# Optimization experiments

Hardware: AMD Instinct MI355X
Metric: run time of the kernel (lower is better)

## Reference

```python
import jax, jax.numpy as jnp
import numpy as np

B, T, C, H, W = 16, 8, 16, 64, 64
HID = 32          # round(sqrt(num_audio_input_ch * num_latent_ch)) = sqrt(16*64)
LAT = 64          # num_latent_ch
K = 3             # kernel_size


def conv(x, w, b):
    # x: [B,Cin,H,W], w: [Cout,Cin,K,K] (OIHW), SAME padding == padding (1,1) for 3x3
    y = jax.lax.conv_general_dilated(x, w, (1, 1), 'SAME',
                                     dimension_numbers=('NCHW', 'OIHW', 'NCHW'))
    return y + b[None, :, None, None]


def lstm_scan(x_seq, w, b, hid):
    # x_seq: [T,B,Cin,H,W] -> hidden sequence [T,B,hid,H,W]
    Bn, Hh, Ww = x_seq.shape[1], x_seq.shape[3], x_seq.shape[4]
    h0 = jnp.zeros((Bn, hid, Hh, Ww), x_seq.dtype)

    def step(carry, x_t):
        h, c = carry
        z = conv(jnp.concatenate([x_t, h], axis=1), w, b)     # [B,4*hid,H,W]
        i, f, o, g = jnp.split(z, 4, axis=1)                   # gate order i,f,o,g
        c2 = jax.nn.sigmoid(f) * c + jax.nn.sigmoid(i) * jnp.tanh(g)
        h2 = jax.nn.sigmoid(o) * jnp.tanh(c2)
        return (h2, c2), h2

    _, hs = jax.lax.scan(step, (h0, h0), x_seq)
    return hs


def bidir_layer(x_seq, wf, bf, wb, bb, hid):
    hf = lstm_scan(x_seq, wf, bf, hid)
    hb = jnp.flip(lstm_scan(jnp.flip(x_seq, 0), wb, bb, hid), 0)
    return jnp.concatenate([hf, hb], axis=2)                   # [T,B,2*hid,H,W]


def setup_inputs() -> dict:
    key = jax.random.key(0)
    ks = jax.random.split(key, 16)
    s = 0.05
    pe_dim = C * H * W
    inp = {
        'x_audio': jax.random.normal(ks[0], (B, T, C, H, W), jnp.float32),
        'midi_notes': jax.random.uniform(ks[1], (B, T, 2), jnp.float32, 0.0, 127.0),
        # note encoder: Linear(2,4) -> ReLU -> Linear(4, C*H*W) -> Tanh
        'enc_w1': jax.random.normal(ks[2], (2, 4), jnp.float32) * s,
        'enc_b1': jnp.zeros((4,), jnp.float32),
        'enc_w2': jax.random.normal(ks[3], (4, pe_dim), jnp.float32) * s,
        'enc_b2': jnp.zeros((pe_dim,), jnp.float32),
        # layer 0 (input C=16), fwd + bwd cells
        'w0f': jax.random.normal(ks[4], (4 * HID, C + HID, K, K), jnp.float32) * s,
        'b0f': jnp.zeros((4 * HID,), jnp.float32),
        'w0b': jax.random.normal(ks[5], (4 * HID, C + HID, K, K), jnp.float32) * s,
        'b0b': jnp.zeros((4 * HID,), jnp.float32),
        # layer 1 (input 2*HID=64)
        'w1f': jax.random.normal(ks[6], (4 * HID, 2 * HID + HID, K, K), jnp.float32) * s,
        'b1f': jnp.zeros((4 * HID,), jnp.float32),
        'w1b': jax.random.normal(ks[7], (4 * HID, 2 * HID + HID, K, K), jnp.float32) * s,
        'b1b': jnp.zeros((4 * HID,), jnp.float32),
        # final conv: 2*HID -> LAT
        'fc_w': jax.random.normal(ks[8], (LAT, 2 * HID, K, K), jnp.float32) * s,
        'fc_b': jnp.zeros((LAT,), jnp.float32),
    }
    return inp


def reference(x_audio, midi_notes, enc_w1, enc_b1, enc_w2, enc_b2,
              w0f, b0f, w0b, b0b, w1f, b1f, w1b, b1b, fc_w, fc_b):
    # positional encoding from MIDI notes, vectorized over all timesteps
    notes = -0.5 + midi_notes / 64.0                              # [B,T,2]
    pe = jnp.tanh(jax.nn.relu(notes @ enc_w1 + enc_b1) @ enc_w2 + enc_b2)  # [B,T,C*H*W]
    x = x_audio + pe.reshape(x_audio.shape)
    xs = jnp.transpose(x, (1, 0, 2, 3, 4))                        # [T,B,C,H,W]
    h = bidir_layer(xs, w0f, b0f, w0b, b0b, HID)                  # [T,B,64,H,W]
    h = bidir_layer(h, w1f, b1f, w1b, b1b, HID)                   # [T,B,64,H,W]
    return conv(h[-1], fc_w, fc_b)                                # [B,LAT,H,W]
```

## Files before the change

kernel.cpp:

```cpp
#include <hip/hip_runtime.h>

typedef _Float16 f16;
typedef _Float16 f16x8 __attribute__((ext_vector_type(8)));
typedef float f32x16 __attribute__((ext_vector_type(16)));

namespace {

constexpr int B_ = 16, T_ = 8, HW = 4096;

__device__ __forceinline__ float sigm(float x)  { return 1.f / (1.f + __expf(-x)); }
__device__ __forceinline__ float ftanh(float x) { return 1.f - 2.f / (1.f + __expf(2.f * x)); }

__device__ __forceinline__ f32x16 zero16() {
  f32x16 v;
#pragma unroll
  for (int i = 0; i < 16; ++i) v[i] = 0.f;
  return v;
}

__device__ __forceinline__ f16x8 zero8h() {
  f16x8 v;
#pragma unroll
  for (int i = 0; i < 8; ++i) v[i] = (f16)0.f;
  return v;
}

struct WSet { const float* src; f16* dst; int KC, NCO, CIN; };

__global__ void warr_kernel(WSet s0, WSet s1, WSet s2, WSet s3, WSet s4) {
  WSet s = s0;
  switch (blockIdx.y) { case 1: s = s1; break; case 2: s = s2; break;
                        case 3: s = s3; break; case 4: s = s4; break; default: break; }
  int n = 9 * s.KC * s.NCO * 16;
  int i = blockIdx.x * 256 + threadIdx.x;
  if (i >= n) return;
  int kk = i & 15;
  int t = i >> 4;
  int co = t % s.NCO;
  int dkc = t / s.NCO;
  int kc = dkc % s.KC, dydx = dkc / s.KC;
  int ci = kc * 16 + kk;
  float v = (ci < s.CIN) ? s.src[(co * s.CIN + ci) * 9 + dydx] : 0.f;
  s.dst[i] = (f16)v;
}

__global__ void pe_kernel(const float* __restrict__ xa, const float* __restrict__ midi,
                          const float* __restrict__ w1, const float* __restrict__ b1,
                          const float* __restrict__ w2, const float* __restrict__ b2,
                          f16* __restrict__ xs) {
  int gid = blockIdx.x * 256 + threadIdx.x;
  int half = gid & 1;
  int gpx = gid >> 1;
  int bt = gpx >> 12, gp = gpx & 4095;
  float n0 = -0.5f + midi[bt * 2 + 0] * (1.f / 64.f);
  float n1 = -0.5f + midi[bt * 2 + 1] * (1.f / 64.f);
  float hk[4];
#pragma unroll
  for (int k = 0; k < 4; ++k)
    hk[k] = fmaxf(fmaf(n0, w1[k], fmaf(n1, w1[4 + k], b1[k])), 0.f);
  f16x8 ov;
#pragma unroll
  for (int j = 0; j < 8; ++j) {
    int c = half * 8 + j;
    long p = (long)c * HW + gp;
    float z = b2[p];
#pragma unroll
    for (int k = 0; k < 4; ++k) z = fmaf(hk[k], w2[(long)k * 65536 + p], z);
    ov[j] = (f16)(xa[(long)bt * 65536 + p] + ftanh(z));
  }
  *reinterpret_cast<f16x8*>(xs + (long)gpx * 16 + half * 8) = ov;
}

struct ConvDir {
  const f16* x;  long xbs;
  const f16* h;  long hbs;
  const f16* w;
  const float* bias;
  const f16* cin;
  f16* cout;
  float* fout;
  f16* hout; long hobs;
};

template<int CIN1, int CIN2, int CINPAD, int KCF, int KC, int HST, int HOST,
         bool GATES, int NCO, int MG>
__global__ __launch_bounds__(512, 4)
void conv_mfma(ConvDir p0, ConvDir p1)
{
  constexpr int NG = 8 / MG;
  constexpr int NF = NCO / (NG * 32);
  constexpr int NPH = 9 * KC;
  constexpr int ACT_BYTES = 180 * CINPAD * 2;
  constexpr int ZB_BYTES  = GATES ? 128 * 128 * 2 : 0;
  constexpr int SMEM = ACT_BYTES > ZB_BYTES ? ACT_BYTES : ZB_BYTES;
  __shared__ __align__(16) char smem[SMEM];
  f16* act = (f16*)smem;
  f16* zls = (f16*)smem;

  const ConvDir P = blockIdx.y ? p1 : p0;
  const int b = blockIdx.z;
  const int tileY = blockIdx.x >> 2, tileX = blockIdx.x & 3;
  const int gy0 = tileY * 8, gx0 = tileX * 16;
  const int tid = threadIdx.x;

  const int lane = tid & 63, wv = tid >> 6;
  const int mg = wv % MG, ng = wv / MG;
  const int rl = lane & 31;
  const int khalf = (lane >> 5) * 8;
  const int laneA = ((rl >> 4) * 18 + (rl & 15)) * CINPAD + khalf;
  const int laneB = rl * 16 + khalf;
  const f16* __restrict__ wng = P.w + laneB + (long)ng * NF * 32 * 16;
  const f16* __restrict__ arow = act + laneA;

  constexpr int UPX = CIN1 / 8, UPH = CIN2 / 8, UPP = UPX + UPH;
  constexpr int NU  = 180 * UPP;
  constexpr int PER = (NU + 511) / 512;
  const bool have_h = (P.h != nullptr);
  f16x8 sreg[PER];
#pragma unroll
  for (int p = 0; p < PER; ++p) {
    sreg[p] = zero8h();
    int i = tid + p * 512;
    if (i < NU) {
      int px = i / UPP, u = i - px * UPP;
      int py = px / 18, pxx = px - py * 18;
      int gy = gy0 + py - 1, gx = gx0 + pxx - 1;
      if ((unsigned)gy < 64u && (unsigned)gx < 64u && (u < UPX || have_h)) {
        long gp = (long)gy * 64 + gx;
        const f16* src = (u < UPX) ? (P.x + b * P.xbs + gp * CIN1 + u * 8)
                                   : (P.h + b * P.hbs + gp * HST + (u - UPX) * 8);
        sreg[p] = *reinterpret_cast<const f16x8*>(src);
      }
    }
  }

  f16x8 bfr[2][NF];
  f16x8 afr[2];

  auto LBF = [&](int ph) {
    const int slot = ph & 1;
    const int dydx = ph / KC, kc = ph % KC;
#pragma unroll
    for (int nf = 0; nf < NF; ++nf)
      bfr[slot][nf] = *reinterpret_cast<const f16x8*>(
          wng + ((long)(dydx * KCF + kc) * NCO + nf * 32) * 16);
  };
  auto LAF = [&](int ph) {
    const int slot = ph & 1;
    const int dydx = ph / KC, kc = ph % KC;
    const int dy = dydx / 3, dx = dydx % 3;
    afr[slot] = *reinterpret_cast<const f16x8*>(
        arow + dx * CINPAD + ((mg * 2 + dy) * 18) * CINPAD + kc * 16);
  };

  LBF(0);
  if (NPH > 1) LBF(1);

#pragma unroll
  for (int p = 0; p < PER; ++p) {
    int i = tid + p * 512;
    if (i < NU) {
      int px = i / UPP, u = i - px * UPP;
      *reinterpret_cast<f16x8*>(act + px * CINPAD + u * 8) = sreg[p];
    }
  }
  __syncthreads();

  f32x16 acc[NF];
#pragma unroll
  for (int nf = 0; nf < NF; ++nf) acc[nf] = zero16();

  LAF(0);
#pragma unroll
  for (int ph = 0; ph < NPH; ++ph) {
    const int slot = ph & 1;
    if (ph + 1 < NPH) LAF(ph + 1);
#pragma unroll
    for (int nf = 0; nf < NF; ++nf)
      acc[nf] = __builtin_amdgcn_mfma_f32_32x32x16_f16(afr[slot], bfr[slot][nf], acc[nf], 0, 0, 0);
    if (ph + 2 < NPH) LBF(ph + 2);
  }

  __syncthreads();

  if constexpr (GATES) {
#pragma unroll
    for (int nf = 0; nf < NF; ++nf) {
      const int col = (ng * NF + nf) * 32 + rl;
      const float bs = P.bias[col];
#pragma unroll
      for (int r = 0; r < 16; ++r) {
        int row = (r & 3) + 8 * (r >> 2) + 4 * (lane >> 5);
        zls[(mg * 32 + row) * 128 + col] = (f16)(acc[nf][r] + bs);
      }
    }
    __syncthreads();
    const int q = tid & 3, px = tid >> 2;
    const int py = px >> 4, pxx = px & 15;
    const long gp = (long)(gy0 + py) * 64 + (gx0 + pxx);
    const f16* zb = zls + px * 128 + q * 8;
    f16x8 zi8 = *reinterpret_cast<const f16x8*>(zb);
    f16x8 zf8 = *reinterpret_cast<const f16x8*>(zb + 32);
    f16x8 zo8 = *reinterpret_cast<const f16x8*>(zb + 64);
    f16x8 zg8 = *reinterpret_cast<const f16x8*>(zb + 96);
    const long cbase = ((long)b * HW + gp) * 32 + q * 8;
    f16x8 c8 = P.cin ? *reinterpret_cast<const f16x8*>(P.cin + cbase) : zero8h();
    f16x8 c2v, h2v;
#pragma unroll
    for (int j = 0; j < 8; ++j) {
      float c2 = sigm((float)zf8[j]) * (float)c8[j]
               + sigm((float)zi8[j]) * ftanh((float)zg8[j]);
      c2v[j] = (f16)c2;
      h2v[j] = (f16)(sigm((float)zo8[j]) * ftanh(c2));
    }
    if (P.cout) *reinterpret_cast<f16x8*>(P.cout + cbase) = c2v;
    *reinterpret_cast<f16x8*>(P.hout + b * P.hobs + gp * HOST + q * 8) = h2v;
  } else {
#pragma unroll
    for (int nf = 0; nf < NF; ++nf) {
      const int co = (ng * NF + nf) * 32 + rl;
      const float bs = P.bias[co];
#pragma unroll
      for (int r = 0; r < 16; ++r) {
        int row = (r & 3) + 8 * (r >> 2) + 4 * (lane >> 5);
        int pxt = mg * 32 + row;
        int py = pxt >> 4, pxx = pxt & 15;
        long gp = (long)(gy0 + py) * 64 + (gx0 + pxx);
        P.fout[((long)b * NCO + co) * HW + gp] = acc[nf][r] + bs;
      }
    }
  }
}

}

extern "C" void kernel_launch(void* const* d_in, const int* in_sizes, int n_in,
                              void* d_out, int out_size, void* d_ws, size_t ws_size,
                              hipStream_t stream) {
  const float* x_audio = (const float*)d_in[0];
  const float* midi    = (const float*)d_in[1];
  const float* enc_w1  = (const float*)d_in[2];
  const float* enc_b1  = (const float*)d_in[3];
  const float* enc_w2  = (const float*)d_in[4];
  const float* enc_b2  = (const float*)d_in[5];
  const float* w0f = (const float*)d_in[6];
  const float* b0f = (const float*)d_in[7];
  const float* w0b = (const float*)d_in[8];
  const float* b0b = (const float*)d_in[9];
  const float* w1f = (const float*)d_in[10];
  const float* b1f = (const float*)d_in[11];
  const float* w1b = (const float*)d_in[12];
  const float* b1b = (const float*)d_in[13];
  const float* fcw = (const float*)d_in[14];
  const float* fcb = (const float*)d_in[15];

  char* ws = (char*)d_ws;
  size_t off = 0;
  auto alloc = [&](size_t bytes) { char* p = ws + off; off += (bytes + 255) & ~(size_t)255; return p; };

  f16* xs    = (f16*)alloc((size_t)B_ * T_ * HW * 16 * 2);
  f16* seq0  = (f16*)alloc((size_t)T_ * B_ * HW * 64 * 2);
  f16* c0f   = (f16*)alloc((size_t)B_ * HW * 32 * 2);
  f16* c0b   = (f16*)alloc((size_t)B_ * HW * 32 * 2);
  f16* c1f   = (f16*)alloc((size_t)B_ * HW * 32 * 2);
  f16* h1p0  = (f16*)alloc((size_t)B_ * HW * 32 * 2);
  f16* h1p1  = (f16*)alloc((size_t)B_ * HW * 32 * 2);
  f16* h1bw  = (f16*)alloc((size_t)B_ * HW * 32 * 2);
  f16* wt0f  = (f16*)alloc((size_t)9 * 3 * 128 * 16 * 2);
  f16* wt0b  = (f16*)alloc((size_t)9 * 3 * 128 * 16 * 2);
  f16* wt1f  = (f16*)alloc((size_t)9 * 6 * 128 * 16 * 2);
  f16* wt1b  = (f16*)alloc((size_t)9 * 6 * 128 * 16 * 2);
  f16* wtfc  = (f16*)alloc((size_t)9 * 4 * 64 * 16 * 2);

  {
    WSet s0{w0f, wt0f, 3, 128, 48}, s1{w0b, wt0b, 3, 128, 48};
    WSet s2{w1f, wt1f, 6, 128, 96}, s3{w1b, wt1b, 6, 128, 96};
    WSet s4{fcw, wtfc, 4, 64, 64};
    warr_kernel<<<dim3(432, 5), 256, 0, stream>>>(s0, s1, s2, s3, s4);
  }

  pe_kernel<<<(B_ * T_ * HW * 2) / 256, 256, 0, stream>>>(
      x_audio, midi, enc_w1, enc_b1, enc_w2, enc_b2, xs);

  const long XSB  = (long)T_ * HW * 16;
  const long SLAB = (long)B_ * HW * 64;
  const long SB   = (long)HW * 64;
  const long HB   = (long)HW * 32;

  {
    ConvDir f{xs, XSB, nullptr, SB, wt0f, b0f, nullptr, c0f, nullptr, seq0, SB};
    ConvDir r{xs + (long)7 * HW * 16, XSB, nullptr, SB, wt0b, b0b, nullptr, c0b,
              nullptr, seq0 + (long)7 * SLAB + 32, SB};
    conv_mfma<16, 32, 56, 3, 1, 64, 64, true, 128, 4>
        <<<dim3(32, 2, 16), 512, 0, stream>>>(f, r);
  }
  for (int s = 1; s < 8; ++s) {
    int tf = s, tb = 7 - s;
    ConvDir f{xs + (long)tf * HW * 16, XSB,
              seq0 + (long)(tf - 1) * SLAB, SB,
              wt0f, b0f, c0f, (s == 7) ? nullptr : c0f, nullptr,
              seq0 + (long)tf * SLAB, SB};
    ConvDir r{xs + (long)tb * HW * 16, XSB,
              seq0 + (long)(tb + 1) * SLAB + 32, SB,
              wt0b, b0b, c0b, (s == 7) ? nullptr : c0b, nullptr,
              seq0 + (long)tb * SLAB + 32, SB};
    conv_mfma<16, 32, 56, 3, 3, 64, 64, true, 128, 4>
        <<<dim3(32, 2, 16), 512, 0, stream>>>(f, r);
  }

  {
    ConvDir f{seq0, SB, nullptr, HB, wt1f, b1f, nullptr, c1f, nullptr, h1p0, HB};
    ConvDir r{seq0 + 7 * SLAB, SB, nullptr, HB, wt1b, b1b, nullptr, nullptr, nullptr, h1bw, HB};
    conv_mfma<64, 32, 104, 6, 4, 32, 32, true, 128, 4>
        <<<dim3(32, 2, 16), 512, 0, stream>>>(f, r);
  }
  for (int s = 1; s < 8; ++s) {
    f16* hprev = (s & 1) ? h1p0 : h1p1;
    f16* hcur  = (s & 1) ? h1p1 : h1p0;
    ConvDir f{seq0 + (long)s * SLAB, SB, hprev, HB, wt1f, b1f,
              c1f, (s == 7) ? nullptr : c1f, nullptr, hcur, HB};
    conv_mfma<64, 32, 104, 6, 6, 32, 32, true, 128, 4>
        <<<dim3(32, 1, 16), 512, 0, stream>>>(f, f);
  }

  {
    ConvDir f{h1p1, HB, h1bw, HB, wtfc, fcb, nullptr, nullptr, (float*)d_out, nullptr, 0};
    conv_mfma<32, 32, 72, 4, 4, 32, 32, false, 64, 4>
        <<<dim3(32, 1, 16), 512, 0, stream>>>(f, f);
  }
}
```

Measured before the change: 490.6 us.

## Halve block to four waves, give each wave two M fragments, triple-buffer weights

The conv kernel now runs 256-thread blocks (4 waves) instead of 512. Each wave computes two 32-pixel M fragments against NCO/64 N fragments, so every weight fragment loaded from global memory is reused across two MFMA tiles. The weight prefetch pipeline is deepened from double to triple buffering. The gate epilogue loops twice per thread to cover all pixels. This trades more registers per wave and fewer waves per block for less redundant weight traffic and better latency hiding.

```diff
diff --git a/kernel.cpp b/kernel.cpp
--- a/kernel.cpp
+++ b/kernel.cpp
@@ -83,12 +83,12 @@
 };
 
 template<int CIN1, int CIN2, int CINPAD, int KCF, int KC, int HST, int HOST,
-         bool GATES, int NCO, int MG>
-__global__ __launch_bounds__(512, 4)
+         bool GATES, int NCO>
+__global__ __launch_bounds__(256, 2)
 void conv_mfma(ConvDir p0, ConvDir p1)
 {
-  constexpr int NG = 8 / MG;
-  constexpr int NF = NCO / (NG * 32);
+  constexpr int MFRAG = 2;
+  constexpr int NF = NCO / 64;
   constexpr int NPH = 9 * KC;
   constexpr int ACT_BYTES = 180 * CINPAD * 2;
   constexpr int ZB_BYTES  = GATES ? 128 * 128 * 2 : 0;
@@ -104,7 +104,7 @@
   const int tid = threadIdx.x;
 
   const int lane = tid & 63, wv = tid >> 6;
-  const int mg = wv % MG, ng = wv / MG;
+  const int mg = wv & 1, ng = wv >> 1;
   const int rl = lane & 31;
   const int khalf = (lane >> 5) * 8;
   const int laneA = ((rl >> 4) * 18 + (rl & 15)) * CINPAD + khalf;
@@ -114,13 +114,13 @@
 
   constexpr int UPX = CIN1 / 8, UPH = CIN2 / 8, UPP = UPX + UPH;
   constexpr int NU  = 180 * UPP;
-  constexpr int PER = (NU + 511) / 512;
+  constexpr int PER = (NU + 255) / 256;
   const bool have_h = (P.h != nullptr);
   f16x8 sreg[PER];
 #pragma unroll
   for (int p = 0; p < PER; ++p) {
     sreg[p] = zero8h();
-    int i = tid + p * 512;
+    int i = tid + p * 256;
     if (i < NU) {
       int px = i / UPP, u = i - px * UPP;
       int py = px / 18, pxx = px - py * 18;
@@ -134,11 +134,11 @@
     }
   }
 
-  f16x8 bfr[2][NF];
-  f16x8 afr[2];
+  f16x8 bfr[3][NF];
+  f16x8 afr[2][MFRAG];
 
   auto LBF = [&](int ph) {
-    const int slot = ph & 1;
+    const int slot = ph % 3;
     const int dydx = ph / KC, kc = ph % KC;
 #pragma unroll
     for (int nf = 0; nf < NF; ++nf)
@@ -149,8 +149,10 @@
     const int slot = ph & 1;
     const int dydx = ph / KC, kc = ph % KC;
     const int dy = dydx / 3, dx = dydx % 3;
-    afr[slot] = *reinterpret_cast<const f16x8*>(
-        arow + dx * CINPAD + ((mg * 2 + dy) * 18) * CINPAD + kc * 16);
+#pragma unroll
+    for (int m = 0; m < MFRAG; ++m)
+      afr[slot][m] = *reinterpret_cast<const f16x8*>(
+          arow + dx * CINPAD + (((mg * MFRAG + m) * 2 + dy) * 18) * CINPAD + kc * 16);
   };
 
   LBF(0);
@@ -158,7 +160,7 @@
 
 #pragma unroll
   for (int p = 0; p < PER; ++p) {
-    int i = tid + p * 512;
+    int i = tid + p * 256;
     if (i < NU) {
       int px = i / UPP, u = i - px * UPP;
       *reinterpret_cast<f16x8*>(act + px * CINPAD + u * 8) = sreg[p];
@@ -166,67 +168,84 @@
   }
   __syncthreads();
 
-  f32x16 acc[NF];
-#pragma unroll
-  for (int nf = 0; nf < NF; ++nf) acc[nf] = zero16();
+  if (NPH > 2) LBF(2);
+
+  f32x16 acc[MFRAG][NF];
+#pragma unroll
+  for (int m = 0; m < MFRAG; ++m)
+#pragma unroll
+    for (int nf = 0; nf < NF; ++nf) acc[m][nf] = zero16();
 
   LAF(0);
 #pragma unroll
   for (int ph = 0; ph < NPH; ++ph) {
-    const int slot = ph & 1;
     if (ph + 1 < NPH) LAF(ph + 1);
 #pragma unroll
-    for (int nf = 0; nf < NF; ++nf)
-      acc[nf] = __builtin_amdgcn_mfma_f32_32x32x16_f16(afr[slot], bfr[slot][nf], acc[nf], 0, 0, 0);
-    if (ph + 2 < NPH) LBF(ph + 2);
+    for (int m = 0; m < MFRAG; ++m)
+#pragma unroll
+      for (int nf = 0; nf < NF; ++nf)
+        acc[m][nf] = __builtin_amdgcn_mfma_f32_32x32x16_f16(
+            afr[ph & 1][m], bfr[ph % 3][nf], acc[m][nf], 0, 0, 0);
+    if (ph + 3 < NPH) LBF(ph + 3);
   }
 
   __syncthreads();
 
   if constexpr (GATES) {
 #pragma unroll
-    for (int nf = 0; nf < NF; ++nf) {
-      const int col = (ng * NF + nf) * 32 + rl;
-      const float bs = P.bias[col];
-#pragma unroll
-      for (int r = 0; r < 16; ++r) {
-        int row = (r & 3) + 8 * (r >> 2) + 4 * (lane >> 5);
-        zls[(mg * 32 + row) * 128 + col] = (f16)(acc[nf][r] + bs);
+    for (int m = 0; m < MFRAG; ++m) {
+#pragma unroll
+      for (int nf = 0; nf < NF; ++nf) {
+        const int col = (ng * NF + nf) * 32 + rl;
+        const float bs = P.bias[col];
+#pragma unroll
+        for (int r = 0; r < 16; ++r) {
+          int row = (r & 3) + 8 * (r >> 2) + 4 * (lane >> 5);
+          int px = (mg * MFRAG + m) * 32 + row;
+          zls[px * 128 + col] = (f16)(acc[m][nf][r] + bs);
+        }
       }
     }
     __syncthreads();
-    const int q = tid & 3, px = tid >> 2;
-    const int py = px >> 4, pxx = px & 15;
-    const long gp = (long)(gy0 + py) * 64 + (gx0 + pxx);
-    const f16* zb = zls + px * 128 + q * 8;
-    f16x8 zi8 = *reinterpret_cast<const f16x8*>(zb);
-    f16x8 zf8 = *reinterpret_cast<const f16x8*>(zb + 32);
-    f16x8 zo8 = *reinterpret_cast<const f16x8*>(zb + 64);
-    f16x8 zg8 = *reinterpret_cast<const f16x8*>(zb + 96);
-    const long cbase = ((long)b * HW + gp) * 32 + q * 8;
-    f16x8 c8 = P.cin ? *reinterpret_cast<const f16x8*>(P.cin + cbase) : zero8h();
-    f16x8 c2v, h2v;
-#pragma unroll
-    for (int j = 0; j < 8; ++j) {
-      float c2 = sigm((float)zf8[j]) * (float)c8[j]
-               + sigm((float)zi8[j]) * ftanh((float)zg8[j]);
-      c2v[j] = (f16)c2;
-      h2v[j] = (f16)(sigm((float)zo8[j]) * ftanh(c2));
-    }
-    if (P.cout) *reinterpret_cast<f16x8*>(P.cout + cbase) = c2v;
-    *reinterpret_cast<f16x8*>(P.hout + b * P.hobs + gp * HOST + q * 8) = h2v;
+#pragma unroll
+    for (int it = 0; it < 2; ++it) {
+      const int idx = tid + it * 256;
+      const int q = idx & 3, px = idx >> 2;
+      const int py = px >> 4, pxx = px & 15;
+      const long gp = (long)(gy0 + py) * 64 + (gx0 + pxx);
+      const f16* zb = zls + px * 128 + q * 8;
+      f16x8 zi8 = *reinterpret_cast<const f16x8*>(zb);
+      f16x8 zf8 = *reinterpret_cast<const f16x8*>(zb + 32);
+      f16x8 zo8 = *reinterpret_cast<const f16x8*>(zb + 64);
+      f16x8 zg8 = *reinterpret_cast<const f16x8*>(zb + 96);
+      const long cbase = ((long)b * HW + gp) * 32 + q * 8;
+      f16x8 c8 = P.cin ? *reinterpret_cast<const f16x8*>(P.cin + cbase) : zero8h();
+      f16x8 c2v, h2v;
+#pragma unroll
+      for (int j = 0; j < 8; ++j) {
+        float c2 = sigm((float)zf8[j]) * (float)c8[j]
+                 + sigm((float)zi8[j]) * ftanh((float)zg8[j]);
+        c2v[j] = (f16)c2;
+        h2v[j] = (f16)(sigm((float)zo8[j]) * ftanh(c2));
+      }
+      if (P.cout) *reinterpret_cast<f16x8*>(P.cout + cbase) = c2v;
+      *reinterpret_cast<f16x8*>(P.hout + b * P.hobs + gp * HOST + q * 8) = h2v;
+    }
   } else {
 #pragma unroll
-    for (int nf = 0; nf < NF; ++nf) {
-      const int co = (ng * NF + nf) * 32 + rl;
-      const float bs = P.bias[co];
-#pragma unroll
-      for (int r = 0; r < 16; ++r) {
-        int row = (r & 3) + 8 * (r >> 2) + 4 * (lane >> 5);
-        int pxt = mg * 32 + row;
-        int py = pxt >> 4, pxx = pxt & 15;
-        long gp = (long)(gy0 + py) * 64 + (gx0 + pxx);
-        P.fout[((long)b * NCO + co) * HW + gp] = acc[nf][r] + bs;
+    for (int m = 0; m < MFRAG; ++m) {
+#pragma unroll
+      for (int nf = 0; nf < NF; ++nf) {
+        const int co = (ng * NF + nf) * 32 + rl;
+        const float bs = P.bias[co];
+#pragma unroll
+        for (int r = 0; r < 16; ++r) {
+          int row = (r & 3) + 8 * (r >> 2) + 4 * (lane >> 5);
+          int pxt = (mg * MFRAG + m) * 32 + row;
+          int py = pxt >> 4, pxx = pxt & 15;
+          long gp = (long)(gy0 + py) * 64 + (gx0 + pxx);
+          P.fout[((long)b * NCO + co) * HW + gp] = acc[m][nf][r] + bs;
+        }
       }
     }
   }
@@ -287,12 +306,14 @@
   const long SB   = (long)HW * 64;
   const long HB   = (long)HW * 32;
 
+  dim3 blk(256);
+
   {
     ConvDir f{xs, XSB, nullptr, SB, wt0f, b0f, nullptr, c0f, nullptr, seq0, SB};
     ConvDir r{xs + (long)7 * HW * 16, XSB, nullptr, SB, wt0b, b0b, nullptr, c0b,
               nullptr, seq0 + (long)7 * SLAB + 32, SB};
-    conv_mfma<16, 32, 56, 3, 1, 64, 64, true, 128, 4>
-        <<<dim3(32, 2, 16), 512, 0, stream>>>(f, r);
+    conv_mfma<16, 32, 56, 3, 1, 64, 64, true, 128>
+        <<<dim3(32, 2, 16), blk, 0, stream>>>(f, r);
   }
   for (int s = 1; s < 8; ++s) {
     int tf = s, tb = 7 - s;
@@ -304,28 +325,28 @@
               seq0 + (long)(tb + 1) * SLAB + 32, SB,
               wt0b, b0b, c0b, (s == 7) ? nullptr : c0b, nullptr,
               seq0 + (long)tb * SLAB + 32, SB};
-    conv_mfma<16, 32, 56, 3, 3, 64, 64, true, 128, 4>
-        <<<dim3(32, 2, 16), 512, 0, stream>>>(f, r);
+    conv_mfma<16, 32, 56, 3, 3, 64, 64, true, 128>
+        <<<dim3(32, 2, 16), blk, 0, stream>>>(f, r);
   }
 
   {
     ConvDir f{seq0, SB, nullptr, HB, wt1f, b1f, nullptr, c1f, nullptr, h1p0, HB};
     ConvDir r{seq0 + 7 * SLAB, SB, nullptr, HB, wt1b, b1b, nullptr, nullptr, nullptr, h1bw, HB};
-    conv_mfma<64, 32, 104, 6, 4, 32, 32, true, 128, 4>
-        <<<dim3(32, 2, 16), 512, 0, stream>>>(f, r);
+    conv_mfma<64, 32, 104, 6, 4, 32, 32, true, 128>
+        <<<dim3(32, 2, 16), blk, 0, stream>>>(f, r);
   }
   for (int s = 1; s < 8; ++s) {
     f16* hprev = (s & 1) ? h1p0 : h1p1;
     f16* hcur  = (s & 1) ? h1p1 : h1p0;
     ConvDir f{seq0 + (long)s * SLAB, SB, hprev, HB, wt1f, b1f,
               c1f, (s == 7) ? nullptr : c1f, nullptr, hcur, HB};
-    conv_mfma<64, 32, 104, 6, 6, 32, 32, true, 128, 4>
-        <<<dim3(32, 1, 16), 512, 0, stream>>>(f, f);
+    conv_mfma<64, 32, 104, 6, 6, 32, 32, true, 128>
+        <<<dim3(32, 1, 16), blk, 0, stream>>>(f, f);
   }
 
   {
     ConvDir f{h1p1, HB, h1bw, HB, wtfc, fcb, nullptr, nullptr, (float*)d_out, nullptr, 0};
-    conv_mfma<32, 32, 72, 4, 4, 32, 32, false, 64, 4>
-        <<<dim3(32, 1, 16), 512, 0, stream>>>(f, f);
-  }
-}
+    conv_mfma<32, 32, 72, 4, 4, 32, 32, false, 64>
+        <<<dim3(32, 1, 16), blk, 0, stream>>>(f, f);
+  }
+}
```

New measurement: 462.8 us, median of 3. 1.06x faster.
